# Kernel tuning notes

Measured on AMD Instinct MI355X. Metric: run time of the kernel, lower is better.

Reference implementation:

```python
import jax, jax.numpy as jnp
import numpy as np


def setup_inputs() -> dict:
    key = jax.random.key(0)
    k1, k2, k3 = jax.random.split(key, 3)
    B, C, H, W = 32, 768, 32, 32
    Cr = 192  # max(1, C // 4)
    x = jax.random.normal(k1, (B, C, H, W), dtype=jnp.float32)
    # 1x1 conv weights flattened to dense matrices (kernel is 1x1)
    w1 = jax.random.normal(k2, (Cr, C), dtype=jnp.float32) * (1.0 / np.sqrt(C))
    b1 = jnp.zeros((Cr,), dtype=jnp.float32)
    w2 = jax.random.normal(k3, (C, Cr), dtype=jnp.float32) * (1.0 / np.sqrt(Cr))
    b2 = jnp.zeros((C,), dtype=jnp.float32)
    return {"x": x, "w1": w1, "b1": b1, "w2": w2, "b2": b2}


def reference(x, w1, b1, w2, b2):
    # Squeeze: global average pool over spatial dims -> [B, C]
    s = jnp.mean(x, axis=(2, 3))
    # Excitation: tiny MLP with swish then sigmoid gate
    h = s @ w1.T + b1                    # [B, Cr]
    h = h * jax.nn.sigmoid(h)            # swish
    g = jax.nn.sigmoid(h @ w2.T + b2)    # [B, C]
    # Scale: broadcast multiply back over the full feature map
    return x * g[:, :, None, None]
```

## Files before the change

kernel.cpp:

```cpp
#include <hip/hip_runtime.h>
#include <math.h>

#define Bn 32
#define Cn 768
#define CRn 192
#define HWn 1024

__global__ __launch_bounds__(256) void se_mean(const float* __restrict__ x,
                                               float* __restrict__ s) {
    const int bc = blockIdx.x;
    const float4* xp = (const float4*)(x + (size_t)bc * HWn);
    float4 v = xp[threadIdx.x];
    float sum = v.x + v.y + v.z + v.w;
    #pragma unroll
    for (int off = 32; off > 0; off >>= 1) sum += __shfl_down(sum, off);
    __shared__ float part[4];
    const int lane = threadIdx.x & 63;
    const int wid  = threadIdx.x >> 6;
    if (lane == 0) part[wid] = sum;
    __syncthreads();
    if (threadIdx.x == 0) {
        s[bc] = (part[0] + part[1] + part[2] + part[3]) * (1.0f / (float)HWn);
    }
}

__global__ __launch_bounds__(256) void se_h(const float* __restrict__ s,
                                            const float* __restrict__ w1,
                                            const float* __restrict__ b1,
                                            float* __restrict__ h) {
    const int wid  = threadIdx.x >> 6;
    const int lane = threadIdx.x & 63;
    const int b = blockIdx.x / (CRn / 4);
    const int j = (blockIdx.x % (CRn / 4)) * 4 + wid;

    const float4* wr = (const float4*)(w1 + (size_t)j * Cn);
    const float4* sp = (const float4*)(s + (size_t)b * Cn);
    float acc = 0.0f;
    #pragma unroll
    for (int t = 0; t < 3; ++t) {
        float4 wv = wr[lane + 64 * t];
        float4 sv = sp[lane + 64 * t];
        acc += wv.x * sv.x + wv.y * sv.y + wv.z * sv.z + wv.w * sv.w;
    }
    #pragma unroll
    for (int off = 32; off > 0; off >>= 1) acc += __shfl_down(acc, off);
    if (lane == 0) {
        float v = acc + b1[j];
        h[b * CRn + j] = v / (1.0f + expf(-v));
    }
}

__global__ __launch_bounds__(256) void se_scale_g(const float* __restrict__ x,
                                                  const float* __restrict__ h,
                                                  const float* __restrict__ w2,
                                                  const float* __restrict__ b2,
                                                  float* __restrict__ out) {
    const int bc = blockIdx.x;
    const int b = bc / Cn;
    const int c = bc % Cn;

    const float4* xp = (const float4*)(x + (size_t)bc * HWn);
    float4* op = (float4*)(out + (size_t)bc * HWn);
    float4 v = xp[threadIdx.x];

    __shared__ float gs;
    if (threadIdx.x < 64) {
        const int lane = threadIdx.x;
        const float* hp = h  + (size_t)b * CRn;
        const float* wp = w2 + (size_t)c * CRn;
        float acc = 0.0f;
        #pragma unroll
        for (int t = 0; t < 3; ++t) {
            acc += hp[lane + 64 * t] * wp[lane + 64 * t];
        }
        #pragma unroll
        for (int off = 32; off > 0; off >>= 1) acc += __shfl_down(acc, off);
        if (lane == 0) {
            float z = acc + b2[c];
            gs = 1.0f / (1.0f + expf(-z));
        }
    }
    __syncthreads();
    const float gv = gs;
    v.x *= gv; v.y *= gv; v.z *= gv; v.w *= gv;
    op[threadIdx.x] = v;
}

extern "C" void kernel_launch(void* const* d_in, const int* in_sizes, int n_in,
                              void* d_out, int out_size, void* d_ws, size_t ws_size,
                              hipStream_t stream) {
    const float* x  = (const float*)d_in[0];
    const float* w1 = (const float*)d_in[1];
    const float* b1 = (const float*)d_in[2];
    const float* w2 = (const float*)d_in[3];
    const float* b2 = (const float*)d_in[4];
    float* out = (float*)d_out;

    float* s = (float*)d_ws;
    float* h = s + (size_t)Bn * Cn;

    se_mean   <<<Bn * Cn,        256, 0, stream>>>(x, s);
    se_h      <<<Bn * (CRn / 4), 256, 0, stream>>>(s, w1, b1, h);
    se_scale_g<<<Bn * Cn,        256, 0, stream>>>(x, h, w2, b2, out);
}
```

Before: 195.4 us.

## Fuse SE stages into one cooperative persistent kernel with grid syncs

Replaces the three launches (mean, hidden MLP, gate+scale) with one cooperative kernel of 1024 persistent blocks that loops over rows per wave and separates the stages with grid-wide syncs. Each wave now handles a whole 1024-element row, so the block-level shared-memory reductions are gone and launch overhead is lower. In exchange it adds two grid barriers and per-wave strided loops with less parallelism per row. Whether x stays in cache between the first and third passes depends on cache size.

```diff
diff --git a/kernel.cpp b/kernel.cpp
--- a/kernel.cpp
+++ b/kernel.cpp
@@ -1,89 +1,88 @@
 #include <hip/hip_runtime.h>
+#include <hip/hip_cooperative_groups.h>
 #include <math.h>
 
-#define Bn 32
-#define Cn 768
-#define CRn 192
-#define HWn 1024
+namespace cg = cooperative_groups;
 
-__global__ __launch_bounds__(256) void se_mean(const float* __restrict__ x,
-                                               float* __restrict__ s) {
-    const int bc = blockIdx.x;
-    const float4* xp = (const float4*)(x + (size_t)bc * HWn);
-    float4 v = xp[threadIdx.x];
-    float sum = v.x + v.y + v.z + v.w;
+#define Bn   32
+#define Cn   768
+#define CRn  192
+#define HWn  1024
+#define ROWS (Bn * Cn)
+#define NBLK 1024
+#define NWAVE (NBLK * 4)
+
+__device__ __forceinline__ float wave_sum_bcast(float v) {
     #pragma unroll
-    for (int off = 32; off > 0; off >>= 1) sum += __shfl_down(sum, off);
-    __shared__ float part[4];
-    const int lane = threadIdx.x & 63;
-    const int wid  = threadIdx.x >> 6;
-    if (lane == 0) part[wid] = sum;
-    __syncthreads();
-    if (threadIdx.x == 0) {
-        s[bc] = (part[0] + part[1] + part[2] + part[3]) * (1.0f / (float)HWn);
-    }
+    for (int off = 32; off > 0; off >>= 1) v += __shfl_xor(v, off);
+    return v;
 }
 
-__global__ __launch_bounds__(256) void se_h(const float* __restrict__ s,
-                                            const float* __restrict__ w1,
-                                            const float* __restrict__ b1,
-                                            float* __restrict__ h) {
-    const int wid  = threadIdx.x >> 6;
+__global__ __launch_bounds__(256, 4) void se_fused(const float* __restrict__ x,
+                                                   const float* __restrict__ w1,
+                                                   const float* __restrict__ b1,
+                                                   const float* __restrict__ w2,
+                                                   const float* __restrict__ b2,
+                                                   float* __restrict__ out,
+                                                   float* __restrict__ s,
+                                                   float* __restrict__ h) {
+    cg::grid_group grid = cg::this_grid();
     const int lane = threadIdx.x & 63;
-    const int b = blockIdx.x / (CRn / 4);
-    const int j = (blockIdx.x % (CRn / 4)) * 4 + wid;
+    const int w    = (blockIdx.x * blockDim.x + threadIdx.x) >> 6;
 
-    const float4* wr = (const float4*)(w1 + (size_t)j * Cn);
-    const float4* sp = (const float4*)(s + (size_t)b * Cn);
-    float acc = 0.0f;
-    #pragma unroll
-    for (int t = 0; t < 3; ++t) {
-        float4 wv = wr[lane + 64 * t];
-        float4 sv = sp[lane + 64 * t];
-        acc += wv.x * sv.x + wv.y * sv.y + wv.z * sv.z + wv.w * sv.w;
+    for (int r = w; r < ROWS; r += NWAVE) {
+        const float4* xp = (const float4*)(x + (size_t)r * HWn);
+        float sum = 0.0f;
+        #pragma unroll
+        for (int t = 0; t < 4; ++t) {
+            float4 v = xp[lane + 64 * t];
+            sum += v.x + v.y + v.z + v.w;
+        }
+        sum = wave_sum_bcast(sum);
+        if (lane == 0) s[r] = sum * (1.0f / (float)HWn);
     }
-    #pragma unroll
-    for (int off = 32; off > 0; off >>= 1) acc += __shfl_down(acc, off);
-    if (lane == 0) {
-        float v = acc + b1[j];
-        h[b * CRn + j] = v / (1.0f + expf(-v));
-    }
-}
+    grid.sync();
 
-__global__ __launch_bounds__(256) void se_scale_g(const float* __restrict__ x,
-                                                  const float* __restrict__ h,
-                                                  const float* __restrict__ w2,
-                                                  const float* __restrict__ b2,
-                                                  float* __restrict__ out) {
-    const int bc = blockIdx.x;
-    const int b = bc / Cn;
-    const int c = bc % Cn;
-
-    const float4* xp = (const float4*)(x + (size_t)bc * HWn);
-    float4* op = (float4*)(out + (size_t)bc * HWn);
-    float4 v = xp[threadIdx.x];
-
-    __shared__ float gs;
-    if (threadIdx.x < 64) {
-        const int lane = threadIdx.x;
-        const float* hp = h  + (size_t)b * CRn;
-        const float* wp = w2 + (size_t)c * CRn;
+    for (int d = w; d < Bn * CRn; d += NWAVE) {
+        const int b = d / CRn;
+        const int j = d % CRn;
+        const float4* wr = (const float4*)(w1 + (size_t)j * Cn);
+        const float4* sp = (const float4*)(s + (size_t)b * Cn);
         float acc = 0.0f;
         #pragma unroll
         for (int t = 0; t < 3; ++t) {
-            acc += hp[lane + 64 * t] * wp[lane + 64 * t];
+            float4 wv = wr[lane + 64 * t];
+            float4 sv = sp[lane + 64 * t];
+            acc += wv.x * sv.x + wv.y * sv.y + wv.z * sv.z + wv.w * sv.w;
         }
-        #pragma unroll
-        for (int off = 32; off > 0; off >>= 1) acc += __shfl_down(acc, off);
+        acc = wave_sum_bcast(acc);
         if (lane == 0) {
-            float z = acc + b2[c];
-            gs = 1.0f / (1.0f + expf(-z));
+            float z = acc + b1[j];
+            h[d] = z / (1.0f + expf(-z));
         }
     }
-    __syncthreads();
-    const float gv = gs;
-    v.x *= gv; v.y *= gv; v.z *= gv; v.w *= gv;
-    op[threadIdx.x] = v;
+    grid.sync();
+
+    for (int r = w; r < ROWS; r += NWAVE) {
+        const int b = r / Cn;
+        const int c = r % Cn;
+        const float* hp = h  + (size_t)b * CRn;
+        const float* wp = w2 + (size_t)c * CRn;
+        float acc = hp[lane]        * wp[lane]
+                  + hp[lane + 64]   * wp[lane + 64]
+                  + hp[lane + 128]  * wp[lane + 128];
+        acc = wave_sum_bcast(acc);
+        const float g = 1.0f / (1.0f + expf(-(acc + b2[c])));
+
+        const float4* xp = (const float4*)(x   + (size_t)r * HWn);
+        float4*       op = (float4*)      (out + (size_t)r * HWn);
+        #pragma unroll
+        for (int t = 0; t < 4; ++t) {
+            float4 v = xp[lane + 64 * t];
+            v.x *= g; v.y *= g; v.z *= g; v.w *= g;
+            op[lane + 64 * t] = v;
+        }
+    }
 }
 
 extern "C" void kernel_launch(void* const* d_in, const int* in_sizes, int n_in,
@@ -97,9 +96,10 @@
     float* out = (float*)d_out;
 
     float* s = (float*)d_ws;
-    float* h = s + (size_t)Bn * Cn;
+    float* h = s + ROWS;
 
-    se_mean   <<<Bn * Cn,        256, 0, stream>>>(x, s);
-    se_h      <<<Bn * (CRn / 4), 256, 0, stream>>>(s, w1, b1, h);
-    se_scale_g<<<Bn * Cn,        256, 0, stream>>>(x, h, w2, b2, out);
+    void* args[] = { (void*)&x, (void*)&w1, (void*)&b1, (void*)&w2, (void*)&b2,
+                     (void*)&out, (void*)&s, (void*)&h };
+    hipLaunchCooperativeKernel((void*)se_fused, dim3(NBLK), dim3(256),
+                               args, 0, stream);
 }
```

Measured after the change: 393.7 us. 2.01x slower.
